# Optimization experiments

Measured on AMD Instinct MI355X. Metric: run time of the kernel, lower is better.

## Reference

```python
import jax, jax.numpy as jnp
import numpy as np

B, K, N, E, T = 4096, 64, 100000, 128, 3


def setup_inputs() -> dict:
    key = jax.random.key(0)
    ks = jax.random.split(key, 16)
    f = lambda i, shape: jax.random.normal(ks[i], shape, dtype=jnp.float32) * 0.05
    return dict(
        nodes=jax.random.randint(ks[0], (B,), 0, N),
        neigh_idx=jax.random.randint(ks[1], (T, B, K), 0, N),
        node_emb=f(2, (N, E)),
        node_prof=f(3, (N, E)),
        neigh_emb=f(4, (T, N, E)),
        neigh_prof=f(5, (T, N, E)),
        W_f=f(6, (2 * E, E)), b_f=jnp.zeros((E,), jnp.float32),
        Wa1=f(7, (2 * E, E)), ba1=jnp.zeros((E,), jnp.float32),
        Wa2=f(8, (E, E)), ba2=jnp.zeros((E,), jnp.float32),
        Wa3=f(9, (E, 1)), ba3=jnp.zeros((1,), jnp.float32),
        W1=f(10, (E, E)), b1=jnp.zeros((E,), jnp.float32),
        W2=f(11, (E, E)), b2=jnp.zeros((E,), jnp.float32),
        Wc=f(12, (2 * E, E)), bc=jnp.zeros((E,), jnp.float32),
        Wt=f(13, (T * E, T)),
    )


def reference(nodes, neigh_idx, node_emb, node_prof, neigh_emb, neigh_prof,
              W_f, b_f, Wa1, ba1, Wa2, ba2, Wa3, ba3,
              W1, b1, W2, b2, Wc, bc, Wt):
    # fusion(emb, profile) = relu(Linear(concat(emb, profile)))
    fuse = lambda e, p: jax.nn.relu(jnp.concatenate([e, p], -1) @ W_f + b_f)

    nodes_fusion = fuse(node_emb[nodes], node_prof[nodes])            # [B,E]

    per_type = []
    for t in range(T):                                                 # small fixed loop over types
        idx = neigh_idx[t]                                             # [B,K]
        nf = fuse(neigh_emb[t][idx], neigh_prof[t][idx])               # [B,K,E]
        # attention MLP over (neighbor, node) pairs -> softmax over K neighbors
        x = jnp.concatenate(
            [nf, jnp.broadcast_to(nodes_fusion[:, None, :], nf.shape)], -1)  # [B,K,2E]
        h = jax.nn.relu(x @ Wa1 + ba1)
        h = jax.nn.relu(h @ Wa2 + ba2)
        att = jax.nn.softmax((h @ Wa3 + ba3).squeeze(-1), axis=1)      # [B,K]
        agg = jnp.einsum('bke,bk->be', nf, att)                        # weighted neighbor sum
        per_type.append(jax.nn.relu(agg @ W1 + b1))                    # linear_1 + relu

    type_agg = jnp.concatenate(per_type, axis=1)                       # [B,T*E]
    att_t = jax.nn.softmax(type_agg @ Wt, axis=1)                      # [B,T]
    final = jnp.einsum('bte,bt->be', type_agg.reshape(B, T, E), att_t)
    final = jax.nn.relu(final @ W2 + b2)                               # linear_2 + relu
    out = jax.nn.relu(jnp.concatenate([nodes_fusion, final], 1) @ Wc + bc)
    return out, att_t[:, :, None]
```

## Files before the change

kernel.cpp:

```cpp
#include <hip/hip_runtime.h>
#include <hip/hip_bf16.h>

#define B_ 4096
#define K_ 64
#define N_ 100000
#define E_ 128
#define T_ 3

typedef __bf16 bf16x8 __attribute__((ext_vector_type(8)));
typedef float  f32x4  __attribute__((ext_vector_type(4)));

static __device__ __forceinline__ bf16x8 cvt8r(f32x4 u, f32x4 v) {
    bf16x8 o;
    o[0] = (__bf16)u[0]; o[1] = (__bf16)u[1]; o[2] = (__bf16)u[2]; o[3] = (__bf16)u[3];
    o[4] = (__bf16)v[0]; o[5] = (__bf16)v[1]; o[6] = (__bf16)v[2]; o[7] = (__bf16)v[3];
    return o;
}

typedef const __attribute__((address_space(1))) void GAS;
typedef __attribute__((address_space(3))) void LAS;
static __device__ __forceinline__ void gload16(const void* g, void* l) {
    __builtin_amdgcn_global_load_lds((GAS*)g, (LAS*)l, 16, 0, 0);
}

#define MFMA16(a, b, c) __builtin_amdgcn_mfma_f32_16x16x32_bf16((a), (b), (c), 0, 0, 0)

__global__ __launch_bounds__(256)
void k_prep(const float* __restrict__ W_f, const float* __restrict__ Wa1,
            const float* __restrict__ Wa2, const float* __restrict__ W1,
            __bf16* __restrict__ WtF, __bf16* __restrict__ Wa1t,
            __bf16* __restrict__ Wa2t, __bf16* __restrict__ W1t) {
    const int n = blockIdx.x;
    const int k = threadIdx.x;
    if (blockIdx.y == 0) {
        WtF[n * 256 + k] = (__bf16)W_f[k * 128 + n];
    } else if (blockIdx.y == 1) {
        if (k < 128) Wa1t[n * 128 + k] = (__bf16)Wa1[k * 128 + n];
    } else if (blockIdx.y == 2) {
        if (k < 128) Wa2t[n * 128 + k] = (__bf16)Wa2[k * 128 + n];
    } else {
        if (k < 128) W1t[n * 128 + k] = (__bf16)W1[k * 128 + n];
    }
}

__global__ __launch_bounds__(128)
void k_node_fusion(const int* __restrict__ nodes,
                   const float* __restrict__ node_emb,
                   const float* __restrict__ node_prof,
                   const float* __restrict__ W_f, const float* __restrict__ b_f,
                   __bf16* __restrict__ nodes_fusion) {
    __shared__ float x[256];
    const int b = blockIdx.x;
    const int e = threadIdx.x;
    const int nd = nodes[b];
    x[e]       = node_emb[(size_t)nd * E_ + e];
    x[128 + e] = node_prof[(size_t)nd * E_ + e];
    __syncthreads();
    float acc = b_f[e];
#pragma unroll 8
    for (int i = 0; i < 256; ++i) acc = fmaf(x[i], W_f[i * E_ + e], acc);
    nodes_fusion[(size_t)b * E_ + e] = (__bf16)fmaxf(acc, 0.f);
}

__global__ __launch_bounds__(128)
void k_node_pre(const __bf16* __restrict__ nodes_fusion,
                const float* __restrict__ Wa1, const float* __restrict__ ba1,
                __bf16* __restrict__ node_pre) {
    __shared__ float x[128];
    const int b = blockIdx.x;
    const int c = threadIdx.x;
    x[c] = (float)nodes_fusion[(size_t)b * E_ + c];
    __syncthreads();
    float acc = ba1[c];
#pragma unroll 8
    for (int i = 0; i < 128; ++i) acc = fmaf(x[i], Wa1[(128 + i) * E_ + c], acc);
    node_pre[(size_t)b * E_ + c] = (__bf16)acc;
}

#define NF_GRID 768
#define NF_TPT (N_ / 16)
#define NF_NJOB (NF_TPT * T_)

__global__ __launch_bounds__(256, 3)
void k_nf(const float* __restrict__ neigh_emb,
          const float* __restrict__ neigh_prof,
          const __bf16* __restrict__ WtF, const float* __restrict__ b_f,
          const __bf16* __restrict__ Wa1t,
          __bf16* __restrict__ NFt, __bf16* __restrict__ Gt) {
    __shared__ __align__(16) float  Xf[2][16 * 256];
    __shared__ __align__(16) __bf16 NFl[16 * 128];

    const int tid  = threadIdx.x;
    const int wid  = tid >> 6, lane = tid & 63;
    const int lr   = lane & 15, lk = lane >> 4;

    bf16x8 wf[16];
#pragma unroll
    for (int ks = 0; ks < 8; ++ks)
#pragma unroll
        for (int n = 0; n < 2; ++n)
            wf[ks * 2 + n] = *(const bf16x8*)&WtF[
                (size_t)(wid * 32 + n * 16 + lr) * 256 + ks * 32 + lk * 8];
    bf16x8 wa1r[8];
#pragma unroll
    for (int ks = 0; ks < 4; ++ks)
#pragma unroll
        for (int n = 0; n < 2; ++n)
            wa1r[ks * 2 + n] = *(const bf16x8*)&Wa1t[
                (size_t)(wid * 32 + n * 16 + lr) * 128 + ks * 32 + lk * 8];
    const float bb0 = b_f[wid * 32 + lr];
    const float bb1 = b_f[wid * 32 + 16 + lr];

    auto stage = [&](int j, int buf) {
        const int t    = j / NF_TPT;
        const int base = (j - t * NF_TPT) * 16;
        const float* embT  = neigh_emb  + (size_t)t * N_ * E_;
        const float* profT = neigh_prof + (size_t)t * N_ * E_;
#pragma unroll
        for (int i = 0; i < 4; ++i) {
            const int r  = wid * 4 + i;
            const int id = base + r;
            const int g  = lane ^ (r & 15);
            const float* src = (g < 32)
                ? embT  + (size_t)id * E_ + g * 4
                : profT + (size_t)id * E_ + (g - 32) * 4;
            gload16(src, (char*)&Xf[buf][0] + r * 1024);
        }
    };

    int job = blockIdx.x;
    stage(job, 0);
    int cur = 0;
    bool first = true;

    const int rr = tid >> 4, qq = tid & 15;
    const int pp = qq ^ rr;

    for (; job < NF_NJOB; job += NF_GRID) {
        const int tc    = job / NF_TPT;
        const int basec = (job - tc * NF_TPT) * 16;

        if (first) { asm volatile("s_waitcnt vmcnt(0)" ::: "memory"); first = false; }
        else       { asm volatile("s_waitcnt vmcnt(2)" ::: "memory"); }
        __builtin_amdgcn_s_barrier();
        __builtin_amdgcn_sched_barrier(0);

        const int nxt = job + NF_GRID;
        if (nxt < NF_NJOB) stage(nxt, cur ^ 1);

        const float* X = &Xf[cur][0];

        {
            f32x4 acc1[2] = {};
#pragma unroll
            for (int ks = 0; ks < 8; ++ks) {
                const int g0 = ks * 8 + lk * 2;
                const f32x4 u0 = *(const f32x4*)&X[lr * 256 + ((g0 ^ lr) << 2)];
                const f32x4 v0 = *(const f32x4*)&X[lr * 256 + (((g0 + 1) ^ lr) << 2)];
                const bf16x8 a0 = cvt8r(u0, v0);
                acc1[0] = MFMA16(a0, wf[ks * 2 + 0], acc1[0]);
                acc1[1] = MFMA16(a0, wf[ks * 2 + 1], acc1[1]);
            }
#pragma unroll
            for (int n = 0; n < 2; ++n) {
                const int c = wid * 32 + n * 16 + lr;
                const float bb = n ? bb1 : bb0;
                const int q = c >> 3, eo = c & 7;
#pragma unroll
                for (int j = 0; j < 4; ++j) {
                    const int rN = lk * 4 + j;
                    NFl[rN * 128 + ((q ^ rN) << 3) + eo] =
                        (__bf16)fmaxf(acc1[n][j] + bb, 0.f);
                }
            }
        }
        asm volatile("s_waitcnt lgkmcnt(0)" ::: "memory");
        __builtin_amdgcn_s_barrier();
        __builtin_amdgcn_sched_barrier(0);

        {
            __bf16* outp = NFt + ((size_t)tc * N_ + basec + rr) * E_ + qq * 8;
            *(bf16x8*)outp = *(const bf16x8*)&NFl[rr * 128 + (pp << 3)];
        }

        {
            f32x4 g[2] = {};
#pragma unroll
            for (int ks = 0; ks < 4; ++ks) {
                const int q = ks * 4 + lk;
                const bf16x8 a = *(const bf16x8*)&NFl[lr * 128 + ((q ^ lr) << 3)];
                g[0] = MFMA16(a, wa1r[ks * 2 + 0], g[0]);
                g[1] = MFMA16(a, wa1r[ks * 2 + 1], g[1]);
            }
            __bf16* Gl = (__bf16*)&Xf[cur][0];
#pragma unroll
            for (int n = 0; n < 2; ++n) {
                const int c = wid * 32 + n * 16 + lr;
                const int q = c >> 3, eo = c & 7;
#pragma unroll
                for (int j = 0; j < 4; ++j) {
                    const int rN = lk * 4 + j;
                    Gl[rN * 128 + ((q ^ rN) << 3) + eo] = (__bf16)g[n][j];
                }
            }
        }
        asm volatile("s_waitcnt lgkmcnt(0)" ::: "memory");
        __builtin_amdgcn_s_barrier();
        __builtin_amdgcn_sched_barrier(0);

        {
            const __bf16* Gl = (const __bf16*)&Xf[cur][0];
            __bf16* outp = Gt + ((size_t)tc * N_ + basec + rr) * E_ + qq * 8;
            *(bf16x8*)outp = *(const bf16x8*)&Gl[rr * 128 + (pp << 3)];
        }
        cur ^= 1;
    }
}

#define ATT_JPB 4
#define ATT_GRID ((B_ * T_) / ATT_JPB)

__global__ __launch_bounds__(256, 3)
void k_att(const int* __restrict__ neigh_idx,
           const __bf16* __restrict__ NFt,
           const __bf16* __restrict__ Gt,
           const __bf16* __restrict__ Wa2t,
           const float* __restrict__ ba2,
           const float* __restrict__ Wa3, const float* __restrict__ ba3,
           const __bf16* __restrict__ node_pre,
           __bf16* __restrict__ aggB) {
    __shared__ __align__(16) __bf16 Gb[2][64 * 128];
    __shared__ __align__(16) __bf16 Nb[64 * 128];
    __shared__ int    idxL[ATT_JPB * 64];
    __shared__ __bf16 npreL[ATT_JPB * 128];
    __shared__ float  scp[128];
    __shared__ float  red4[512];

    const int tid = threadIdx.x;
    const int wid = tid >> 6, lane = tid & 63;
    const int lr = lane & 15, lk = lane >> 4;
    const int job0 = blockIdx.x * ATT_JPB;
    const int t    = job0 / B_;
    const int b0   = job0 % B_;

    const __bf16* NFtab = NFt + (size_t)t * N_ * E_;
    const __bf16* Gtab  = Gt  + (size_t)t * N_ * E_;

    const int mp = wid >> 1, h = wid & 1;
    bf16x8 wa2r[4][4];
    float ba2r[4], wa3r[4];
#pragma unroll
    for (int n = 0; n < 4; ++n) {
        const int col = h * 64 + n * 16 + lr;
#pragma unroll
        for (int ks = 0; ks < 4; ++ks)
            wa2r[ks][n] = *(const bf16x8*)&Wa2t[(size_t)col * 128 + ks * 32 + lk * 8];
        ba2r[n] = ba2[col];
        wa3r[n] = Wa3[col];
    }
    const float ba3v = ba3[0];

    idxL[tid] = neigh_idx[(size_t)job0 * K_ + tid];
#pragma unroll
    for (int i = tid; i < ATT_JPB * 128; i += 256) {
        const int jj = i >> 7, c = i & 127;
        npreL[i] = node_pre[(size_t)(b0 + jj) * E_ + c];
    }
    __syncthreads();

    auto stage = [&](const __bf16* tab, int jj, char* dst) {
#pragma unroll
        for (int i = 0; i < 4; ++i) {
            const int rowblock = wid * 16 + i * 4;
            const int rsub = i * 4 + (lane >> 4);
            const int q = (lane & 15) ^ rsub;
            const int id = idxL[jj * 64 + wid * 16 + rsub];
            gload16(tab + (size_t)id * E_ + q * 8, dst + rowblock * 256);
        }
    };

    stage(Gtab, 0, (char*)&Gb[0][0]);

    for (int it = 0; it < ATT_JPB; ++it) {
        if (it == 0) { asm volatile("s_waitcnt vmcnt(0)" ::: "memory"); }
        else         { asm volatile("s_waitcnt vmcnt(1)" ::: "memory"); }
        __builtin_amdgcn_s_barrier();
        __builtin_amdgcn_sched_barrier(0);

        stage(NFtab, it, (char*)&Nb[0]);
        if (it + 1 < ATT_JPB) stage(Gtab, it + 1, (char*)&Gb[(it + 1) & 1][0]);

        const __bf16* GbC = &Gb[it & 1][0];

        f32x4 acc[2][4] = {};
#pragma unroll
        for (int ks = 0; ks < 4; ++ks) {
            const int q = ks * 4 + lk;
            const bf16x8 g0 = *(const bf16x8*)&GbC[(32 * mp + lr) * 128 + ((q ^ lr) << 3)];
            const bf16x8 g1 = *(const bf16x8*)&GbC[(32 * mp + 16 + lr) * 128 + ((q ^ lr) << 3)];
            const bf16x8 np = *(const bf16x8*)&npreL[it * 128 + q * 8];
            bf16x8 a0, a1;
#pragma unroll
            for (int j = 0; j < 8; ++j) {
                const float nv = (float)np[j];
                a0[j] = (__bf16)fmaxf((float)g0[j] + nv, 0.f);
                a1[j] = (__bf16)fmaxf((float)g1[j] + nv, 0.f);
            }
#pragma unroll
            for (int n = 0; n < 4; ++n) {
                acc[0][n] = MFMA16(a0, wa2r[ks][n], acc[0][n]);
                acc[1][n] = MFMA16(a1, wa2r[ks][n], acc[1][n]);
            }
        }

#pragma unroll
        for (int mi = 0; mi < 2; ++mi)
#pragma unroll
            for (int j = 0; j < 4; ++j) {
                float v = 0.f;
#pragma unroll
                for (int n = 0; n < 4; ++n)
                    v += fmaxf(acc[mi][n][j] + ba2r[n], 0.f) * wa3r[n];
                v += __shfl_xor(v, 1);
                v += __shfl_xor(v, 2);
                v += __shfl_xor(v, 4);
                v += __shfl_xor(v, 8);
                if (lr == 0)
                    scp[h * 64 + 32 * mp + mi * 16 + lk * 4 + j] = v;
            }
        asm volatile("s_waitcnt lgkmcnt(0)" ::: "memory");
        __builtin_amdgcn_s_barrier();
        __builtin_amdgcn_sched_barrier(0);

        float att;
        {
            const float v = scp[lane] + scp[64 + lane] + ba3v;
            float m = v;
#pragma unroll
            for (int o = 32; o > 0; o >>= 1) m = fmaxf(m, __shfl_xor(m, o));
            const float pe = __expf(v - m);
            float s = pe;
#pragma unroll
            for (int o = 32; o > 0; o >>= 1) s += __shfl_xor(s, o);
            att = pe / s;
        }

        if (it + 1 < ATT_JPB) { asm volatile("s_waitcnt vmcnt(4)" ::: "memory"); }
        else                  { asm volatile("s_waitcnt vmcnt(0)" ::: "memory"); }
        __builtin_amdgcn_sched_barrier(0);

        {
            float p0 = 0.f, p1 = 0.f;
            const int q0 = lane >> 3, eo = lane & 7;
            const int q1 = (lane + 64) >> 3;
#pragma unroll
            for (int i = 0; i < 16; ++i) {
                const int row = wid * 16 + i;
                const float av = __shfl(att, row);
                p0 = fmaf(av, (float)Nb[row * 128 + ((q0 ^ (row & 15)) << 3) + eo], p0);
                p1 = fmaf(av, (float)Nb[row * 128 + ((q1 ^ (row & 15)) << 3) + eo], p1);
            }
            red4[wid * 128 + lane] = p0;
            red4[wid * 128 + 64 + lane] = p1;
        }
        asm volatile("s_waitcnt lgkmcnt(0)" ::: "memory");
        __builtin_amdgcn_s_barrier();
        __builtin_amdgcn_sched_barrier(0);

        if (lane < 32) {
            const int e = wid * 32 + lane;
            const float s = red4[e] + red4[128 + e] + red4[256 + e] + red4[384 + e];
            aggB[((size_t)(b0 + it) * T_ + t) * E_ + e] = (__bf16)s;
        }
    }
}

__global__ __launch_bounds__(256)
void k_w1(const __bf16* __restrict__ aggB, const __bf16* __restrict__ W1t,
          const float* __restrict__ b1, __bf16* __restrict__ type_agg) {
    const int tid  = threadIdx.x;
    const int wid  = tid >> 6;
    const int lane = tid & 63;
    const int lr   = lane & 15;
    const int lk   = lane >> 4;
    const int rbase = blockIdx.x * 64 + wid * 16;

    f32x4 acc[8] = {};
#pragma unroll
    for (int ks = 0; ks < 4; ++ks) {
        const bf16x8 a = *(const bf16x8*)&aggB[(size_t)(rbase + lr) * 128 + ks * 32 + lk * 8];
        const __bf16* wb = W1t + (size_t)lr * 128 + ks * 32 + lk * 8;
#pragma unroll
        for (int n = 0; n < 8; ++n) {
            const bf16x8 w = *(const bf16x8*)(wb + (size_t)n * 16 * 128);
            acc[n] = MFMA16(a, w, acc[n]);
        }
    }
#pragma unroll
    for (int n = 0; n < 8; ++n) {
        const int col = n * 16 + lr;
        const float bb = b1[col];
#pragma unroll
        for (int j = 0; j < 4; ++j) {
            const int row = rbase + lk * 4 + j;
            type_agg[(size_t)row * 128 + col] = (__bf16)fmaxf(acc[n][j] + bb, 0.f);
        }
    }
}

__global__ __launch_bounds__(128)
void k_final(const __bf16* __restrict__ type_agg,
             const __bf16* __restrict__ nodes_fusion,
             const float* __restrict__ Wt,
             const float* __restrict__ W2, const float* __restrict__ b2,
             const float* __restrict__ Wc, const float* __restrict__ bc,
             float* __restrict__ out, float* __restrict__ att_out) {
    __shared__ float ta[384];
    __shared__ float nfu[128];
    __shared__ float fin[128];
    __shared__ float hb[128];
    __shared__ float att[3];
    __shared__ float red[3][128];

    const int b = blockIdx.x;
    const int e = threadIdx.x;

    const float v0 = (float)type_agg[(size_t)b * 384 + e];
    const float v1 = (float)type_agg[(size_t)b * 384 + 128 + e];
    const float v2 = (float)type_agg[(size_t)b * 384 + 256 + e];
    ta[e] = v0; ta[128 + e] = v1; ta[256 + e] = v2;
    nfu[e] = (float)nodes_fusion[(size_t)b * E_ + e];

    float p0, p1, p2;
    {
        const float* w0 = Wt + (size_t)e * 3;
        const float* w1 = Wt + (size_t)(128 + e) * 3;
        const float* w2 = Wt + (size_t)(256 + e) * 3;
        p0 = v0 * w0[0] + v1 * w1[0] + v2 * w2[0];
        p1 = v0 * w0[1] + v1 * w1[1] + v2 * w2[1];
        p2 = v0 * w0[2] + v1 * w1[2] + v2 * w2[2];
    }
    red[0][e] = p0; red[1][e] = p1; red[2][e] = p2;
    __syncthreads();

    if (e < 3) {
        float s = 0.f;
        for (int i = 0; i < 128; ++i) s += red[e][i];
        red[e][0] = s;
    }
    __syncthreads();
    if (e == 0) {
        const float s0 = red[0][0], s1 = red[1][0], s2 = red[2][0];
        const float m  = fmaxf(s0, fmaxf(s1, s2));
        const float e0 = __expf(s0 - m), e1 = __expf(s1 - m), e2 = __expf(s2 - m);
        const float inv = 1.f / (e0 + e1 + e2);
        att[0] = e0 * inv; att[1] = e1 * inv; att[2] = e2 * inv;
    }
    __syncthreads();

    fin[e] = att[0] * ta[e] + att[1] * ta[128 + e] + att[2] * ta[256 + e];
    __syncthreads();

    float acc = b2[e];
#pragma unroll 8
    for (int i = 0; i < 128; ++i) acc = fmaf(fin[i], W2[i * E_ + e], acc);
    hb[e] = fmaxf(acc, 0.f);
    __syncthreads();

    float acc2 = bc[e];
#pragma unroll 8
    for (int i = 0; i < 128; ++i) acc2 = fmaf(nfu[i], Wc[i * E_ + e], acc2);
#pragma unroll 8
    for (int i = 0; i < 128; ++i) acc2 = fmaf(hb[i], Wc[(128 + i) * E_ + e], acc2);
    out[(size_t)b * E_ + e] = fmaxf(acc2, 0.f);

    if (e < 3) att_out[(size_t)b * 3 + e] = att[e];
}

extern "C" void kernel_launch(void* const* d_in, const int* in_sizes, int n_in,
                              void* d_out, int out_size, void* d_ws, size_t ws_size,
                              hipStream_t stream) {
    const int*   nodes      = (const int*)d_in[0];
    const int*   neigh_idx  = (const int*)d_in[1];
    const float* node_emb   = (const float*)d_in[2];
    const float* node_prof  = (const float*)d_in[3];
    const float* neigh_emb  = (const float*)d_in[4];
    const float* neigh_prof = (const float*)d_in[5];
    const float* W_f = (const float*)d_in[6];  const float* b_f = (const float*)d_in[7];
    const float* Wa1 = (const float*)d_in[8];  const float* ba1 = (const float*)d_in[9];
    const float* Wa2 = (const float*)d_in[10]; const float* ba2 = (const float*)d_in[11];
    const float* Wa3 = (const float*)d_in[12]; const float* ba3 = (const float*)d_in[13];
    const float* W1  = (const float*)d_in[14]; const float* b1  = (const float*)d_in[15];
    const float* W2  = (const float*)d_in[16]; const float* b2  = (const float*)d_in[17];
    const float* Wc  = (const float*)d_in[18]; const float* bc  = (const float*)d_in[19];
    const float* Wt  = (const float*)d_in[20];

    float* out     = (float*)d_out;
    float* att_out = out + (size_t)B_ * E_;

    char* ws = (char*)d_ws;
    __bf16* nodes_fusion = (__bf16*)(ws);
    __bf16* node_pre     = (__bf16*)(ws + (1u << 20));
    __bf16* type_agg     = (__bf16*)(ws + (2u << 20));
    __bf16* aggB         = (__bf16*)(ws + (5u << 20));
    __bf16* WtF          = (__bf16*)(ws + (8u << 20));
    __bf16* Wa1t         = (__bf16*)(ws + (8u << 20) + 65536);
    __bf16* Wa2t         = (__bf16*)(ws + (8u << 20) + 98304);
    __bf16* W1t          = (__bf16*)(ws + (8u << 20) + 131072);
    __bf16* NFt          = (__bf16*)(ws + (9u << 20));
    __bf16* Gt           = (__bf16*)(ws + (83u << 20));

    k_prep<<<dim3(128, 4), 256, 0, stream>>>(W_f, Wa1, Wa2, W1, WtF, Wa1t, Wa2t, W1t);
    k_node_fusion<<<B_, 128, 0, stream>>>(nodes, node_emb, node_prof, W_f, b_f,
                                          nodes_fusion);
    k_node_pre<<<B_, 128, 0, stream>>>(nodes_fusion, Wa1, ba1, node_pre);
    k_nf<<<NF_GRID, 256, 0, stream>>>(neigh_emb, neigh_prof, WtF, b_f, Wa1t,
                                      NFt, Gt);
    k_att<<<ATT_GRID, 256, 0, stream>>>(neigh_idx, NFt, Gt, Wa2t, ba2,
                                        Wa3, ba3, node_pre, aggB);
    k_w1<<<(B_ * T_) / 64, 256, 0, stream>>>(aggB, W1t, b1, type_agg);
    k_final<<<B_, 128, 0, stream>>>(type_agg, nodes_fusion, Wt, W2, b2, Wc, bc,
                                    out, att_out);
}
```

Baseline: 328.1 us.

## Process one (node,type) job per attention block instead of pipelined four

The attention kernel changes from four jobs per block, with a double-buffered gather pipeline and per-block weight registers, to one job per block on a 2D grid. Both gathered tables are loaded at once, Wa2 is read from global/cache inside the MFMA loop, and the weighted neighbor sum is reduced with one shuffle instead of an LDS cross-wave pass. The intent is to cut LDS use and registers so more blocks fit per CU (launch bound raised to 4), hiding latency through occupancy rather than software pipelining. In exchange, each block reloads Wa2 and node_pre, and the overlap between gather and compute within a block is lost.

```diff
diff --git a/kernel.cpp b/kernel.cpp
--- a/kernel.cpp
+++ b/kernel.cpp
@@ -217,10 +217,7 @@
     }
 }
 
-#define ATT_JPB 4
-#define ATT_GRID ((B_ * T_) / ATT_JPB)
-
-__global__ __launch_bounds__(256, 3)
+__global__ __launch_bounds__(256, 4)
 void k_att(const int* __restrict__ neigh_idx,
            const __bf16* __restrict__ NFt,
            const __bf16* __restrict__ Gt,
@@ -229,90 +226,65 @@
            const float* __restrict__ Wa3, const float* __restrict__ ba3,
            const __bf16* __restrict__ node_pre,
            __bf16* __restrict__ aggB) {
-    __shared__ __align__(16) __bf16 Gb[2][64 * 128];
+    __shared__ __align__(16) __bf16 Gb[64 * 128];
     __shared__ __align__(16) __bf16 Nb[64 * 128];
-    __shared__ int    idxL[ATT_JPB * 64];
-    __shared__ __bf16 npreL[ATT_JPB * 128];
+    __shared__ __bf16 npreL[128];
     __shared__ float  scp[128];
-    __shared__ float  red4[512];
-
+
+    const int b   = blockIdx.x;
+    const int t   = blockIdx.y;
     const int tid = threadIdx.x;
     const int wid = tid >> 6, lane = tid & 63;
     const int lr = lane & 15, lk = lane >> 4;
-    const int job0 = blockIdx.x * ATT_JPB;
-    const int t    = job0 / B_;
-    const int b0   = job0 % B_;
-
+
+    const int idv = neigh_idx[((size_t)t * B_ + b) * K_ + wid * 16 + lr];
+
+    const __bf16* Gtab  = Gt  + (size_t)t * N_ * E_;
     const __bf16* NFtab = NFt + (size_t)t * N_ * E_;
-    const __bf16* Gtab  = Gt  + (size_t)t * N_ * E_;
+#pragma unroll
+    for (int i = 0; i < 4; ++i) {
+        const int rowblock = wid * 16 + i * 4;
+        const int rsub = i * 4 + (lane >> 4);
+        const int q = (lane & 15) ^ rsub;
+        const int id = __shfl(idv, rsub);
+        gload16(Gtab  + (size_t)id * E_ + q * 8, (char*)Gb + rowblock * 256);
+        gload16(NFtab + (size_t)id * E_ + q * 8, (char*)Nb + rowblock * 256);
+    }
+    if (tid < 128) npreL[tid] = node_pre[(size_t)b * E_ + tid];
+    __syncthreads();
 
     const int mp = wid >> 1, h = wid & 1;
-    bf16x8 wa2r[4][4];
-    float ba2r[4], wa3r[4];
-#pragma unroll
-    for (int n = 0; n < 4; ++n) {
-        const int col = h * 64 + n * 16 + lr;
-#pragma unroll
-        for (int ks = 0; ks < 4; ++ks)
-            wa2r[ks][n] = *(const bf16x8*)&Wa2t[(size_t)col * 128 + ks * 32 + lk * 8];
-        ba2r[n] = ba2[col];
-        wa3r[n] = Wa3[col];
-    }
-    const float ba3v = ba3[0];
-
-    idxL[tid] = neigh_idx[(size_t)job0 * K_ + tid];
-#pragma unroll
-    for (int i = tid; i < ATT_JPB * 128; i += 256) {
-        const int jj = i >> 7, c = i & 127;
-        npreL[i] = node_pre[(size_t)(b0 + jj) * E_ + c];
-    }
-    __syncthreads();
-
-    auto stage = [&](const __bf16* tab, int jj, char* dst) {
-#pragma unroll
-        for (int i = 0; i < 4; ++i) {
-            const int rowblock = wid * 16 + i * 4;
-            const int rsub = i * 4 + (lane >> 4);
-            const int q = (lane & 15) ^ rsub;
-            const int id = idxL[jj * 64 + wid * 16 + rsub];
-            gload16(tab + (size_t)id * E_ + q * 8, dst + rowblock * 256);
-        }
-    };
-
-    stage(Gtab, 0, (char*)&Gb[0][0]);
-
-    for (int it = 0; it < ATT_JPB; ++it) {
-        if (it == 0) { asm volatile("s_waitcnt vmcnt(0)" ::: "memory"); }
-        else         { asm volatile("s_waitcnt vmcnt(1)" ::: "memory"); }
-        __builtin_amdgcn_s_barrier();
-        __builtin_amdgcn_sched_barrier(0);
-
-        stage(NFtab, it, (char*)&Nb[0]);
-        if (it + 1 < ATT_JPB) stage(Gtab, it + 1, (char*)&Gb[(it + 1) & 1][0]);
-
-        const __bf16* GbC = &Gb[it & 1][0];
-
-        f32x4 acc[2][4] = {};
-#pragma unroll
-        for (int ks = 0; ks < 4; ++ks) {
-            const int q = ks * 4 + lk;
-            const bf16x8 g0 = *(const bf16x8*)&GbC[(32 * mp + lr) * 128 + ((q ^ lr) << 3)];
-            const bf16x8 g1 = *(const bf16x8*)&GbC[(32 * mp + 16 + lr) * 128 + ((q ^ lr) << 3)];
-            const bf16x8 np = *(const bf16x8*)&npreL[it * 128 + q * 8];
-            bf16x8 a0, a1;
-#pragma unroll
-            for (int j = 0; j < 8; ++j) {
-                const float nv = (float)np[j];
-                a0[j] = (__bf16)fmaxf((float)g0[j] + nv, 0.f);
-                a1[j] = (__bf16)fmaxf((float)g1[j] + nv, 0.f);
-            }
-#pragma unroll
-            for (int n = 0; n < 4; ++n) {
-                acc[0][n] = MFMA16(a0, wa2r[ks][n], acc[0][n]);
-                acc[1][n] = MFMA16(a1, wa2r[ks][n], acc[1][n]);
-            }
-        }
-
+    f32x4 acc[2][4] = {};
+#pragma unroll
+    for (int ks = 0; ks < 4; ++ks) {
+        const int q = ks * 4 + lk;
+        const bf16x8 g0 = *(const bf16x8*)&Gb[(32 * mp + lr) * 128 + ((q ^ lr) << 3)];
+        const bf16x8 g1 = *(const bf16x8*)&Gb[(32 * mp + 16 + lr) * 128 + ((q ^ lr) << 3)];
+        const bf16x8 np = *(const bf16x8*)&npreL[q * 8];
+        bf16x8 a0, a1;
+#pragma unroll
+        for (int j = 0; j < 8; ++j) {
+            const float nv = (float)np[j];
+            a0[j] = (__bf16)fmaxf((float)g0[j] + nv, 0.f);
+            a1[j] = (__bf16)fmaxf((float)g1[j] + nv, 0.f);
+        }
+        const __bf16* wb = Wa2t + (size_t)(h * 64 + lr) * 128 + ks * 32 + lk * 8;
+#pragma unroll
+        for (int n = 0; n < 4; ++n) {
+            const bf16x8 w = *(const bf16x8*)(wb + (size_t)n * 16 * 128);
+            acc[0][n] = MFMA16(a0, w, acc[0][n]);
+            acc[1][n] = MFMA16(a1, w, acc[1][n]);
+        }
+    }
+
+    {
+        float ba2r[4], wa3r[4];
+#pragma unroll
+        for (int n = 0; n < 4; ++n) {
+            const int col = h * 64 + n * 16 + lr;
+            ba2r[n] = ba2[col];
+            wa3r[n] = Wa3[col];
+        }
 #pragma unroll
         for (int mi = 0; mi < 2; ++mi)
 #pragma unroll
@@ -328,50 +300,36 @@
                 if (lr == 0)
                     scp[h * 64 + 32 * mp + mi * 16 + lk * 4 + j] = v;
             }
-        asm volatile("s_waitcnt lgkmcnt(0)" ::: "memory");
-        __builtin_amdgcn_s_barrier();
-        __builtin_amdgcn_sched_barrier(0);
-
-        float att;
-        {
-            const float v = scp[lane] + scp[64 + lane] + ba3v;
-            float m = v;
-#pragma unroll
-            for (int o = 32; o > 0; o >>= 1) m = fmaxf(m, __shfl_xor(m, o));
-            const float pe = __expf(v - m);
-            float s = pe;
-#pragma unroll
-            for (int o = 32; o > 0; o >>= 1) s += __shfl_xor(s, o);
-            att = pe / s;
-        }
-
-        if (it + 1 < ATT_JPB) { asm volatile("s_waitcnt vmcnt(4)" ::: "memory"); }
-        else                  { asm volatile("s_waitcnt vmcnt(0)" ::: "memory"); }
-        __builtin_amdgcn_sched_barrier(0);
-
-        {
-            float p0 = 0.f, p1 = 0.f;
-            const int q0 = lane >> 3, eo = lane & 7;
-            const int q1 = (lane + 64) >> 3;
-#pragma unroll
-            for (int i = 0; i < 16; ++i) {
-                const int row = wid * 16 + i;
-                const float av = __shfl(att, row);
-                p0 = fmaf(av, (float)Nb[row * 128 + ((q0 ^ (row & 15)) << 3) + eo], p0);
-                p1 = fmaf(av, (float)Nb[row * 128 + ((q1 ^ (row & 15)) << 3) + eo], p1);
-            }
-            red4[wid * 128 + lane] = p0;
-            red4[wid * 128 + 64 + lane] = p1;
-        }
-        asm volatile("s_waitcnt lgkmcnt(0)" ::: "memory");
-        __builtin_amdgcn_s_barrier();
-        __builtin_amdgcn_sched_barrier(0);
-
-        if (lane < 32) {
-            const int e = wid * 32 + lane;
-            const float s = red4[e] + red4[128 + e] + red4[256 + e] + red4[384 + e];
-            aggB[((size_t)(b0 + it) * T_ + t) * E_ + e] = (__bf16)s;
-        }
+    }
+    __syncthreads();
+
+    float att;
+    {
+        const float v = scp[lane] + scp[64 + lane] + ba3[0];
+        float m = v;
+#pragma unroll
+        for (int o = 32; o > 0; o >>= 1) m = fmaxf(m, __shfl_xor(m, o));
+        const float pe = __expf(v - m);
+        float s = pe;
+#pragma unroll
+        for (int o = 32; o > 0; o >>= 1) s += __shfl_xor(s, o);
+        att = pe / s;
+    }
+
+    {
+        const int e = wid * 32 + (lane & 31);
+        const int half = lane >> 5;
+        const int qe = e >> 3, eo = e & 7;
+        float p = 0.f;
+#pragma unroll
+        for (int i = 0; i < 32; ++i) {
+            const int row = half * 32 + i;
+            const float av = __shfl(att, row);
+            p = fmaf(av, (float)Nb[row * 128 + ((qe ^ (row & 15)) << 3) + eo], p);
+        }
+        p += __shfl_xor(p, 32);
+        if (lane < 32)
+            aggB[((size_t)b * T_ + t) * E_ + e] = (__bf16)p;
     }
 }
 
@@ -516,8 +474,8 @@
     k_node_pre<<<B_, 128, 0, stream>>>(nodes_fusion, Wa1, ba1, node_pre);
     k_nf<<<NF_GRID, 256, 0, stream>>>(neigh_emb, neigh_prof, WtF, b_f, Wa1t,
                                       NFt, Gt);
-    k_att<<<ATT_GRID, 256, 0, stream>>>(neigh_idx, NFt, Gt, Wa2t, ba2,
-                                        Wa3, ba3, node_pre, aggB);
+    k_att<<<dim3(B_, T_), 256, 0, stream>>>(neigh_idx, NFt, Gt, Wa2t, ba2,
+                                            Wa3, ba3, node_pre, aggB);
     k_w1<<<(B_ * T_) / 64, 256, 0, stream>>>(aggB, W1t, b1, type_agg);
     k_final<<<B_, 128, 0, stream>>>(type_agg, nodes_fusion, Wt, W2, b2, Wc, bc,
                                     out, att_out);
```

After: 302.8 us. 1.08x faster.
